# Optimization experiments

Measured on AMD Instinct MI355X. Metric: run time of the kernel, lower is better.

The kernel has to match this reference:

```python
import jax, jax.numpy as jnp
import numpy as np

D_MODEL = 1024
N_HEAD = 16
D_HEAD = D_MODEL // N_HEAD
BSZ, QLEN, MLEN = 2, 1024, 1024
KLEN = QLEN + MLEN


def setup_inputs() -> dict:
    key = jax.random.key(0)
    ks = jax.random.split(key, 10)
    s = 1.0 / np.sqrt(D_MODEL)
    inp = {
        "x": jax.random.normal(ks[0], (BSZ, QLEN, D_MODEL), jnp.float32),
        "mem": jax.random.normal(ks[1], (BSZ, MLEN, D_MODEL), jnp.float32),
        "pos_emb": jax.random.normal(ks[2], (KLEN, D_MODEL), jnp.float32),
        # causal mask with memory: query i may attend to key j iff j <= i + MLEN
        "attn_mask": (jnp.arange(KLEN)[None, :] > (jnp.arange(QLEN)[:, None] + MLEN))[None, None],
        "Wq": jax.random.normal(ks[3], (D_MODEL, D_MODEL), jnp.float32) * s,
        "Wk": jax.random.normal(ks[4], (D_MODEL, D_MODEL), jnp.float32) * s,
        "Wv": jax.random.normal(ks[5], (D_MODEL, D_MODEL), jnp.float32) * s,
        "Wr": jax.random.normal(ks[6], (D_MODEL, D_MODEL), jnp.float32) * s,
        "Wo": jax.random.normal(ks[7], (D_MODEL, D_MODEL), jnp.float32) * s,
        "r_w_bias": jax.random.normal(ks[8], (N_HEAD, D_HEAD), jnp.float32) * 0.02,
        "r_r_bias": jax.random.normal(ks[9], (N_HEAD, D_HEAD), jnp.float32) * 0.02,
    }
    return inp


def _rel_shift(x):
    # x: [b, n, q, k]
    b, n, q, k = x.shape
    x_padded = jnp.pad(x, ((0, 0), (0, 0), (0, 0), (1, 0)))  # zero column at front
    x_padded = x_padded.reshape(b, n, k + 1, q)
    return x_padded[:, :, 1:].reshape(b, n, q, k)


def reference(x, mem, pos_emb, attn_mask, Wq, Wk, Wv, Wr, Wo, r_w_bias, r_r_bias):
    bsz, qlen, _ = x.shape
    k_input = jnp.concatenate([mem, x], axis=1)
    klen = k_input.shape[1]
    scale = 1.0 / np.sqrt(D_HEAD)

    # projections -> [b, n, len, d]
    q = jnp.einsum('bqe,de->bqd', x, Wq).reshape(bsz, qlen, N_HEAD, D_HEAD).transpose(0, 2, 1, 3)
    k = jnp.einsum('bke,de->bkd', k_input, Wk).reshape(bsz, klen, N_HEAD, D_HEAD).transpose(0, 2, 1, 3)
    v = jnp.einsum('bke,de->bkd', k_input, Wv).reshape(bsz, klen, N_HEAD, D_HEAD).transpose(0, 2, 1, 3)
    r = jnp.einsum('ke,de->kd', pos_emb, Wr).reshape(klen, N_HEAD, D_HEAD).transpose(1, 0, 2)  # [n,k,d]

    AC = jnp.einsum('bnqd,bnkd->bnqk', q + r_w_bias[None, :, None, :], k)
    BD = jnp.einsum('bnqd,nkd->bnqk', q + r_r_bias[None, :, None, :], r)
    BD = _rel_shift(BD)

    attn_score = (AC + BD) * scale
    attn_score = jnp.where(attn_mask, -jnp.inf, attn_score)
    attn_prob = jax.nn.softmax(attn_score, axis=-1)

    attn_vec = jnp.einsum('bnqk,bnkd->bnqd', attn_prob, v)
    attn_vec = attn_vec.transpose(0, 2, 1, 3).reshape(bsz, qlen, N_HEAD * D_HEAD)
    return jnp.einsum('bqd,ed->bqe', attn_vec, Wo)
```

## Files before the change

kernel.cpp:

```cpp
#include <hip/hip_runtime.h>


#define B_SZ 2
#define QLEN 1024
#define MLEN 1024
#define KLEN 2048
#define DMODEL 1024
#define NH 16
#define DH 64
#define NSPLIT 2

typedef _Float16 f16;
typedef __attribute__((ext_vector_type(8))) _Float16 f16x8;
typedef __attribute__((ext_vector_type(4))) _Float16 f16x4;
typedef __attribute__((ext_vector_type(4))) float f32x4;

__device__ __forceinline__ f16 f2h(float v) { return (f16)v; }
__device__ __forceinline__ float h2f(f16 v) { return (float)v; }
__device__ __forceinline__ float exp2fast(float v) {
  return __builtin_amdgcn_exp2f(v);
}

__device__ __forceinline__ f32x4 mfma16(f16x8 a, f16x8 b, f32x4 c) {
  return __builtin_amdgcn_mfma_f32_16x16x32_f16(a, b, c, 0, 0, 0);
}

__device__ __forceinline__ void gload_lds16(const f16* g, f16* l) {
  __builtin_amdgcn_global_load_lds(
      (const __attribute__((address_space(1))) void*)g,
      (__attribute__((address_space(3))) void*)l, 16, 0, 0);
}

__device__ __forceinline__ float bperm(int srclane, float v) {
  return __int_as_float(
      __builtin_amdgcn_ds_bpermute(srclane << 2, __float_as_int(v)));
}

__global__ __launch_bounds__(256) void convert_kernel(const float* __restrict__ src,
                                                      f16* __restrict__ dst, int n4) {
  const int i = blockIdx.x * 256 + threadIdx.x;
  if (i >= n4) return;
  const float4 v = reinterpret_cast<const float4*>(src)[i];
  f16x4 o = {(f16)v.x, (f16)v.y, (f16)v.z, (f16)v.w};
  reinterpret_cast<f16x4*>(dst)[i] = o;
}

__global__ __launch_bounds__(256) void pack_weights_kernel(
    const float* __restrict__ Wq, const float* __restrict__ Wk,
    const float* __restrict__ Wv, const float* __restrict__ Wr,
    const float* __restrict__ Wo, f16* __restrict__ Wqb, f16* __restrict__ Wkb,
    f16* __restrict__ Wvb, f16* __restrict__ Wrb, f16* __restrict__ Wob) {
  const float* src;
  f16* dst;
  switch (blockIdx.y) {
    case 0: src = Wq; dst = Wqb; break;
    case 1: src = Wk; dst = Wkb; break;
    case 2: src = Wv; dst = Wvb; break;
    case 3: src = Wr; dst = Wrb; break;
    default: src = Wo; dst = Wob; break;
  }
  const int i = blockIdx.x * 256 + threadIdx.x;
  const float4 v = reinterpret_cast<const float4*>(src)[i];
  f16x4 o = {(f16)v.x, (f16)v.y, (f16)v.z, (f16)v.w};
  reinterpret_cast<f16x4*>(dst)[i] = o;
}

__global__ __launch_bounds__(256) void build_kin_kernel(const float* __restrict__ x,
                                                        const float* __restrict__ mem,
                                                        f16* __restrict__ kin,
                                                        f16* __restrict__ xb) {
  const int i = blockIdx.x * 256 + threadIdx.x;
  const int per_b = KLEN * DMODEL / 4;
  const int b = i / per_b;
  const int rem = i - b * per_b;
  const int row = rem / (DMODEL / 4);
  const int cc = (rem - row * (DMODEL / 4)) * 4;
  const float* src = (row < MLEN)
      ? mem + ((size_t)b * MLEN + row) * DMODEL + cc
      : x + ((size_t)b * QLEN + (row - MLEN)) * DMODEL + cc;
  const float4 v = *reinterpret_cast<const float4*>(src);
  f16x4 o = {(f16)v.x, (f16)v.y, (f16)v.z, (f16)v.w};
  *reinterpret_cast<f16x4*>(kin + (size_t)i * 4) = o;
  if (row >= MLEN)
    *reinterpret_cast<f16x4*>(&xb[((size_t)b * QLEN + (row - MLEN)) * DMODEL + cc]) = o;
}

template <int DUAL, int OUT_F32>
__device__ __forceinline__ void gemm_core(const f16* __restrict__ A,
                                          const f16* __restrict__ Bm,
                                          void* __restrict__ C0v,
                                          void* __restrict__ C1v,
                                          const float* __restrict__ bias0,
                                          const float* __restrict__ bias1, int bm,
                                          int bn) {
  const int tid = threadIdx.x;
  const int wave = tid >> 6, lane = tid & 63;
  const int wr = wave >> 1, wc = wave & 1;
  const int lr = lane & 15, hi = lane >> 4;

  __shared__ f16 As[128 * 64];
  __shared__ f16 Bs[128 * 64];

  f32x4 acc[4][4];
#pragma unroll
  for (int m = 0; m < 4; ++m)
#pragma unroll
    for (int n = 0; n < 4; ++n) acc[m][n] = f32x4{0.f, 0.f, 0.f, 0.f};

  for (int k0 = 0; k0 < DMODEL; k0 += 64) {
    __syncthreads();
#pragma unroll
    for (int it = 0; it < 4; ++it) {
      const int c = it * 256 + tid;
      const int row = c >> 3, c16 = c & 7;
      const int c16s = c16 ^ (row & 7);
      gload_lds16(&A[(size_t)(bm + row) * DMODEL + k0 + c16s * 8], &As[c * 8]);
      gload_lds16(&Bm[(size_t)(bn + row) * DMODEL + k0 + c16s * 8], &Bs[c * 8]);
    }
    __syncthreads();
#pragma unroll
    for (int kk = 0; kk < 2; ++kk) {
      f16x8 af[4], bf[4];
#pragma unroll
      for (int m = 0; m < 4; ++m) {
        const int row = wr * 64 + m * 16 + lr;
        const int colf = (kk * 32 + hi * 8) ^ ((row & 7) << 3);
        af[m] = *reinterpret_cast<const f16x8*>(&As[row * 64 + colf]);
      }
#pragma unroll
      for (int n = 0; n < 4; ++n) {
        const int row = wc * 64 + n * 16 + lr;
        const int colf = (kk * 32 + hi * 8) ^ ((row & 7) << 3);
        bf[n] = *reinterpret_cast<const f16x8*>(&Bs[row * 64 + colf]);
      }
#pragma unroll
      for (int m = 0; m < 4; ++m)
#pragma unroll
        for (int n = 0; n < 4; ++n) acc[m][n] = mfma16(af[m], bf[n], acc[m][n]);
    }
  }

#pragma unroll
  for (int m = 0; m < 4; ++m)
#pragma unroll
    for (int n = 0; n < 4; ++n)
#pragma unroll
      for (int r = 0; r < 4; ++r) {
        const int grow = bm + wr * 64 + m * 16 + hi * 4 + r;
        const int gcol = bn + wc * 64 + n * 16 + lr;
        const float v = acc[m][n][r];
        if constexpr (OUT_F32) {
          reinterpret_cast<float*>(C0v)[(size_t)grow * DMODEL + gcol] = v;
        } else if constexpr (DUAL) {
          const float sc = 0.125f * 1.44269504f;
          reinterpret_cast<f16*>(C0v)[(size_t)grow * DMODEL + gcol] =
              f2h((v + bias0[gcol]) * sc);
          reinterpret_cast<f16*>(C1v)[(size_t)grow * DMODEL + gcol] =
              f2h((v + bias1[gcol]) * sc);
        } else {
          reinterpret_cast<f16*>(C0v)[(size_t)grow * DMODEL + gcol] = f2h(v);
        }
      }
}

__global__ __launch_bounds__(256) void proj_kernel(
    const f16* __restrict__ Xb, const f16* __restrict__ Kin,
    const f16* __restrict__ Pos, const f16* __restrict__ Wqb,
    const f16* __restrict__ Wkb, const f16* __restrict__ Wvb,
    const f16* __restrict__ Wrb, f16* __restrict__ Qwb, f16* __restrict__ Qrb,
    f16* __restrict__ Kbb, f16* __restrict__ Vbb, f16* __restrict__ Rbb,
    const float* __restrict__ rwb, const float* __restrict__ rrb) {
  const int y = blockIdx.y;
  const int bn = blockIdx.x * 128;
  if (y < 16) {
    gemm_core<1, 0>(Xb, Wqb, Qwb, Qrb, rwb, rrb, y * 128, bn);
  } else if (y < 48) {
    gemm_core<0, 0>(Kin, Wkb, Kbb, nullptr, nullptr, nullptr, (y - 16) * 128, bn);
  } else if (y < 80) {
    gemm_core<0, 0>(Kin, Wvb, Vbb, nullptr, nullptr, nullptr, (y - 48) * 128, bn);
  } else {
    gemm_core<0, 0>(Pos, Wrb, Rbb, nullptr, nullptr, nullptr, (y - 80) * 128, bn);
  }
}

__global__ __launch_bounds__(256) void gemm_out_kernel(const f16* __restrict__ A,
                                                       const f16* __restrict__ Bm,
                                                       float* __restrict__ C) {
  gemm_core<0, 1>(A, Bm, C, nullptr, nullptr, nullptr, blockIdx.y * 128,
                  blockIdx.x * 128);
}

__global__ __launch_bounds__(512) void attn_kernel(
    const f16* __restrict__ Qw, const f16* __restrict__ Qr,
    const f16* __restrict__ Kb, const f16* __restrict__ Vb,
    const f16* __restrict__ Rb, f16* __restrict__ Opart,
    float2* __restrict__ MLp) {
  const int bid = blockIdx.x;
  const int xcd = bid & 7, rr = bid >> 3;
  const int grp = xcd * 4 + (rr >> 4);
  const int ii = rr & 15;
  const int b = grp >> 4, n = grp & 15;
  const int qi = ii >> 1, split = ii & 1;

  const int qb = qi * 128;
  const int tid = threadIdx.x;
  const int wave = tid >> 6, lane = tid & 63;
  const int lr = lane & 15, hi = lane >> 4;
  const int t0 = hi * 4;
  const int w0 = qb + wave * 16;

  const int T = (qb + 128 + MLEN) >> 6;
  const int jt_beg = split ? (T >> 1) : 0;
  const int jt_end = split ? T : (T >> 1);
  const int wlimit = w0 + 15 + MLEN;

  __shared__ f16 Ks[2][64][72];
  __shared__ f16 Vs[2][64][72];
  __shared__ f16 Ps[8][16][72];

  f16x8 qw[2], qr[2];
  {
    const size_t qbase = ((size_t)(b * QLEN + w0 + lr)) * DMODEL + n * DH;
#pragma unroll
    for (int kk = 0; kk < 2; ++kk) {
      qw[kk] = *reinterpret_cast<const f16x8*>(&Qw[qbase + kk * 32 + hi * 8]);
      qr[kk] = *reinterpret_cast<const f16x8*>(&Qr[qbase + kk * 32 + hi * 8]);
    }
  }

  f32x4 o[4];
#pragma unroll
  for (int df = 0; df < 4; ++df) o[df] = f32x4{0.f, 0.f, 0.f, 0.f};
  float mrow[4], lrow[4];
#pragma unroll
  for (int r = 0; r < 4; ++r) { mrow[r] = -1e30f; lrow[r] = 0.f; }

  const f16* Rn = Rb + n * DH;

  const int krow = tid >> 3, kc8 = (tid & 7) << 3;
  const int vrow = tid & 63, vc8 = ((tid >> 6) & 7) << 3;
  f16x8 kreg, vreg;
  auto issue = [&](int jt) {
    const size_t kvb = ((size_t)(b * KLEN + (jt << 6))) * DMODEL + n * DH;
    kreg = *reinterpret_cast<const f16x8*>(&Kb[kvb + (size_t)krow * DMODEL + kc8]);
    vreg = *reinterpret_cast<const f16x8*>(&Vb[kvb + (size_t)vrow * DMODEL + vc8]);
  };
  auto commit = [&](int p) {
    *reinterpret_cast<f16x8*>(&Ks[p][krow][kc8]) = kreg;
#pragma unroll
    for (int e = 0; e < 8; ++e) Vs[p][vc8 + e][vrow] = vreg[e];
  };

  issue(jt_beg);
  commit(0);
  __syncthreads();
  int p = 0;

  for (int jt = jt_beg; jt < jt_end; ++jt) {
    const bool hn = (jt + 1 < jt_end);
    if (hn) issue(jt + 1);

    const int j0 = jt << 6;

    if (j0 <= wlimit) {
      f32x4 s[4];
#pragma unroll
      for (int nf = 0; nf < 4; ++nf) s[nf] = f32x4{0.f, 0.f, 0.f, 0.f};
#pragma unroll
      for (int kk = 0; kk < 2; ++kk)
#pragma unroll
        for (int nf = 0; nf < 4; ++nf) {
          const f16x8 kf = *reinterpret_cast<const f16x8*>(
              &Ks[p][nf * 16 + lr][kk * 32 + hi * 8]);
          s[nf] = mfma16(qw[kk], kf, s[nf]);
        }

      const int u0 = j0 + QLEN - 16 - w0;
      f32x4 bd[5];
#pragma unroll
      for (int nt = 0; nt < 5; ++nt) bd[nt] = f32x4{0.f, 0.f, 0.f, 0.f};
#pragma unroll
      for (int nt = 0; nt < 5; ++nt) {
        const int u = u0 + nt * 16 + lr;
        const int uc = u < KLEN ? u : KLEN - 1;
#pragma unroll
        for (int kk = 0; kk < 2; ++kk) {
          const f16x8 rf = *reinterpret_cast<const f16x8*>(
              &Rn[(size_t)uc * DMODEL + kk * 32 + hi * 8]);
          bd[nt] = mfma16(qr[kk], rf, bd[nt]);
        }
      }

#pragma unroll
      for (int r = 0; r < 4; ++r) {
        const int off = 15 - t0 - r;
        const int sl = lr + off;
        const int srclane = hi * 16 + (sl & 15);
        const bool cross = sl >= 16;
        const int i = w0 + t0 + r;
#pragma unroll
        for (int nf = 0; nf < 4; ++nf) {
          const float x0 = bperm(srclane, bd[nf][r]);
          const float x1 = bperm(srclane, bd[nf + 1][r]);
          const float bv = cross ? x1 : x0;
          const int j = j0 + nf * 16 + lr;
          s[nf][r] = (j <= i + MLEN) ? (s[nf][r] + bv) : -1e30f;
        }
      }

#pragma unroll
      for (int r = 0; r < 4; ++r) {
        float tmax = fmaxf(fmaxf(s[0][r], s[1][r]), fmaxf(s[2][r], s[3][r]));
#pragma unroll
        for (int d = 1; d < 16; d <<= 1) tmax = fmaxf(tmax, __shfl_xor(tmax, d, 64));
        const float mnew = fmaxf(mrow[r], tmax);
        const float alpha = exp2fast(mrow[r] - mnew);
        mrow[r] = mnew;
        float tsum = 0.f;
#pragma unroll
        for (int nf = 0; nf < 4; ++nf) {
          const float pv = exp2fast(s[nf][r] - mnew);
          s[nf][r] = pv;
          tsum += pv;
        }
#pragma unroll
        for (int d = 1; d < 16; d <<= 1) tsum += __shfl_xor(tsum, d, 64);
        lrow[r] = lrow[r] * alpha + tsum;
#pragma unroll
        for (int df = 0; df < 4; ++df) o[df][r] *= alpha;
      }

#pragma unroll
      for (int nf = 0; nf < 4; ++nf)
#pragma unroll
        for (int r = 0; r < 4; ++r) Ps[wave][t0 + r][nf * 16 + lr] = f2h(s[nf][r]);

#pragma unroll
      for (int kk = 0; kk < 2; ++kk) {
        const f16x8 pa =
            *reinterpret_cast<const f16x8*>(&Ps[wave][lr][kk * 32 + hi * 8]);
#pragma unroll
        for (int df = 0; df < 4; ++df) {
          const f16x8 vb = *reinterpret_cast<const f16x8*>(
              &Vs[p][df * 16 + lr][kk * 32 + hi * 8]);
          o[df] = mfma16(pa, vb, o[df]);
        }
      }
    }

    if (hn) commit(p ^ 1);
    __syncthreads();
    p ^= 1;
  }

  const size_t obase =
      (((size_t)(split * B_SZ + b) * NH + n) * QLEN + w0 + t0) * DH;
#pragma unroll
  for (int df = 0; df < 4; ++df)
#pragma unroll
    for (int r = 0; r < 4; ++r)
      Opart[obase + (size_t)r * DH + df * 16 + lr] = f2h(o[df][r]);
  if (lr == 0) {
    const size_t mbase = ((size_t)(split * B_SZ + b) * NH + n) * QLEN + w0 + t0;
#pragma unroll
    for (int r = 0; r < 4; ++r) MLp[mbase + r] = float2{mrow[r], lrow[r]};
  }
}

__global__ __launch_bounds__(256) void combine_kernel(const f16* __restrict__ Op,
                                                      const float2* __restrict__ ML,
                                                      f16* __restrict__ AV) {
  const int idx = blockIdx.x * 256 + threadIdx.x;
  const int d8 = idx & 7;
  const int i = (idx >> 3) & 1023;
  const int n = (idx >> 13) & 15;
  const int b = idx >> 17;
  size_t rs[NSPLIT];
  float2 ml[NSPLIT];
#pragma unroll
  for (int s = 0; s < NSPLIT; ++s) {
    rs[s] = ((size_t)((s * B_SZ + b) * NH + n)) * QLEN + i;
    ml[s] = ML[rs[s]];
  }
  float M = ml[0].x;
#pragma unroll
  for (int s = 1; s < NSPLIT; ++s) M = fmaxf(M, ml[s].x);
  float es[NSPLIT], l = 0.f;
#pragma unroll
  for (int s = 0; s < NSPLIT; ++s) {
    es[s] = __builtin_amdgcn_exp2f(ml[s].x - M);
    l += ml[s].y * es[s];
  }
  const float inv = 1.f / l;
  float acc[8] = {0, 0, 0, 0, 0, 0, 0, 0};
#pragma unroll
  for (int s = 0; s < NSPLIT; ++s) {
    const f16x8 ov = *reinterpret_cast<const f16x8*>(&Op[rs[s] * DH + d8 * 8]);
#pragma unroll
    for (int e = 0; e < 8; ++e) acc[e] += h2f(ov[e]) * es[s];
  }
  f16x8 outv;
#pragma unroll
  for (int e = 0; e < 8; ++e) outv[e] = f2h(acc[e] * inv);
  *reinterpret_cast<f16x8*>(&AV[((size_t)(b * QLEN + i)) * DMODEL + n * DH + d8 * 8]) =
      outv;
}

extern "C" void kernel_launch(void* const* d_in, const int* in_sizes, int n_in,
                              void* d_out, int out_size, void* d_ws, size_t ws_size,
                              hipStream_t stream) {
  (void)in_sizes; (void)n_in; (void)out_size; (void)ws_size;
  const float* x   = (const float*)d_in[0];
  const float* mem = (const float*)d_in[1];
  const float* pos = (const float*)d_in[2];
  const float* Wq  = (const float*)d_in[4];
  const float* Wk  = (const float*)d_in[5];
  const float* Wv  = (const float*)d_in[6];
  const float* Wr  = (const float*)d_in[7];
  const float* Wo  = (const float*)d_in[8];
  const float* rwb = (const float*)d_in[9];
  const float* rrb = (const float*)d_in[10];
  float* out = (float*)d_out;

  char* ws = (char*)d_ws;
  size_t off = 0;
  auto alloc = [&](size_t bytes) {
    void* p = (void*)(ws + off);
    off += (bytes + 255) & ~(size_t)255;
    return p;
  };
  f16* Xb  = (f16*)alloc((size_t)B_SZ * QLEN * DMODEL * 2);
  f16* Kin = (f16*)alloc((size_t)B_SZ * KLEN * DMODEL * 2);
  f16* Pos = (f16*)alloc((size_t)KLEN * DMODEL * 2);
  f16* Wqb = (f16*)alloc((size_t)DMODEL * DMODEL * 2);
  f16* Wkb = (f16*)alloc((size_t)DMODEL * DMODEL * 2);
  f16* Wvb = (f16*)alloc((size_t)DMODEL * DMODEL * 2);
  f16* Wrb = (f16*)alloc((size_t)DMODEL * DMODEL * 2);
  f16* Wob = (f16*)alloc((size_t)DMODEL * DMODEL * 2);
  f16* Qwb = (f16*)alloc((size_t)B_SZ * QLEN * DMODEL * 2);
  f16* Qrb = (f16*)alloc((size_t)B_SZ * QLEN * DMODEL * 2);
  f16* Kbb = (f16*)alloc((size_t)B_SZ * KLEN * DMODEL * 2);
  f16* Vbb = (f16*)alloc((size_t)B_SZ * KLEN * DMODEL * 2);
  f16* Rbb = (f16*)alloc((size_t)KLEN * DMODEL * 2);
  f16* AVb = (f16*)alloc((size_t)B_SZ * QLEN * DMODEL * 2);
  f16* Opart  = (f16*)alloc((size_t)NSPLIT * B_SZ * NH * QLEN * DH * 2);
  float2* MLp = (float2*)alloc((size_t)NSPLIT * B_SZ * NH * QLEN * 8);

  pack_weights_kernel<<<dim3(1024, 5), dim3(256), 0, stream>>>(
      Wq, Wk, Wv, Wr, Wo, Wqb, Wkb, Wvb, Wrb, Wob);
  convert_kernel<<<dim3(KLEN * DMODEL / 4 / 256), dim3(256), 0, stream>>>(
      pos, Pos, KLEN * DMODEL / 4);
  build_kin_kernel<<<dim3(B_SZ * KLEN * DMODEL / 4 / 256), dim3(256), 0, stream>>>(
      x, mem, Kin, Xb);

  proj_kernel<<<dim3(8, 96), dim3(256), 0, stream>>>(
      Xb, Kin, Pos, Wqb, Wkb, Wvb, Wrb, Qwb, Qrb, Kbb, Vbb, Rbb, rwb, rrb);

  attn_kernel<<<dim3(QLEN / 128 * NSPLIT * NH * B_SZ), dim3(512), 0, stream>>>(
      Qwb, Qrb, Kbb, Vbb, Rbb, Opart, MLp);

  combine_kernel<<<dim3(B_SZ * NH * QLEN * (DH / 8) / 256), dim3(256), 0, stream>>>(
      Opart, MLp, AVb);

  gemm_out_kernel<<<dim3(DMODEL / 128, B_SZ * QLEN / 128), dim3(256), 0, stream>>>(
      AVb, Wob, out);
}
```

Measured before the change: 318.4 us.

## Replace padded double-buffered LDS tiles with XOR-swizzled single buffer

Removes the padding from the K, V and P shared-memory tiles and uses an XOR swizzle on the column index to avoid bank conflicts. K and V drop from double to single buffering, which lowers LDS use per block and may allow more resident blocks. The cost is a second __syncthreads per iteration: the next tile can only be committed after every wave has finished reading the current one, so loads overlap less with compute.

```diff
diff --git a/kernel.cpp b/kernel.cpp
--- a/kernel.cpp
+++ b/kernel.cpp
@@ -208,15 +208,16 @@
   const int lr = lane & 15, hi = lane >> 4;
   const int t0 = hi * 4;
   const int w0 = qb + wave * 16;
+  const int swz = (lr & 7) << 3;
 
   const int T = (qb + 128 + MLEN) >> 6;
   const int jt_beg = split ? (T >> 1) : 0;
   const int jt_end = split ? T : (T >> 1);
   const int wlimit = w0 + 15 + MLEN;
 
-  __shared__ f16 Ks[2][64][72];
-  __shared__ f16 Vs[2][64][72];
-  __shared__ f16 Ps[8][16][72];
+  __shared__ f16 Ks[64][64];
+  __shared__ f16 Vs[64][64];
+  __shared__ f16 Ps[8][16][64];
 
   f16x8 qw[2], qr[2];
   {
@@ -245,16 +246,15 @@
     kreg = *reinterpret_cast<const f16x8*>(&Kb[kvb + (size_t)krow * DMODEL + kc8]);
     vreg = *reinterpret_cast<const f16x8*>(&Vb[kvb + (size_t)vrow * DMODEL + vc8]);
   };
-  auto commit = [&](int p) {
-    *reinterpret_cast<f16x8*>(&Ks[p][krow][kc8]) = kreg;
-#pragma unroll
-    for (int e = 0; e < 8; ++e) Vs[p][vc8 + e][vrow] = vreg[e];
+  auto commit = [&]() {
+    *reinterpret_cast<f16x8*>(&Ks[krow][kc8 ^ ((krow & 7) << 3)]) = kreg;
+#pragma unroll
+    for (int e = 0; e < 8; ++e) Vs[vc8 + e][vrow ^ (e << 3)] = vreg[e];
   };
 
   issue(jt_beg);
-  commit(0);
+  commit();
   __syncthreads();
-  int p = 0;
 
   for (int jt = jt_beg; jt < jt_end; ++jt) {
     const bool hn = (jt + 1 < jt_end);
@@ -271,7 +271,7 @@
 #pragma unroll
         for (int nf = 0; nf < 4; ++nf) {
           const f16x8 kf = *reinterpret_cast<const f16x8*>(
-              &Ks[p][nf * 16 + lr][kk * 32 + hi * 8]);
+              &Ks[nf * 16 + lr][(kk * 32 + hi * 8) ^ swz]);
           s[nf] = mfma16(qw[kk], kf, s[nf]);
         }
 
@@ -333,24 +333,26 @@
 #pragma unroll
       for (int nf = 0; nf < 4; ++nf)
 #pragma unroll
-        for (int r = 0; r < 4; ++r) Ps[wave][t0 + r][nf * 16 + lr] = f2h(s[nf][r]);
+        for (int r = 0; r < 4; ++r)
+          Ps[wave][t0 + r][(nf * 16 + lr) ^ (((t0 + r) & 7) << 3)] =
+              f2h(s[nf][r]);
 
 #pragma unroll
       for (int kk = 0; kk < 2; ++kk) {
-        const f16x8 pa =
-            *reinterpret_cast<const f16x8*>(&Ps[wave][lr][kk * 32 + hi * 8]);
+        const f16x8 pa = *reinterpret_cast<const f16x8*>(
+            &Ps[wave][lr][(kk * 32 + hi * 8) ^ swz]);
 #pragma unroll
         for (int df = 0; df < 4; ++df) {
           const f16x8 vb = *reinterpret_cast<const f16x8*>(
-              &Vs[p][df * 16 + lr][kk * 32 + hi * 8]);
+              &Vs[df * 16 + lr][(kk * 32 + hi * 8) ^ swz]);
           o[df] = mfma16(pa, vb, o[df]);
         }
       }
     }
 
-    if (hn) commit(p ^ 1);
     __syncthreads();
-    p ^= 1;
+    if (hn) commit();
+    __syncthreads();
   }
 
   const size_t obase =
```

Result: no change. 313.4 us (-1.6%).
